# Kernel tuning notes

Hardware: AMD Instinct MI355X
Metric: run time of the kernel (lower is better)

## Reference

```python
import jax, jax.numpy as jnp
import numpy as np
from jax import lax

NF = 64
KS = 3
PAD = 1
TOPK = 2
DG = 8          # deformable_groups
N = KS * KS     # 9 sampling points


def conv3x3(x, w, b):
    y = lax.conv_general_dilated(x, w, (1, 1), 'SAME',
                                 dimension_numbers=('NCHW', 'OIHW', 'NCHW'))
    return y + b[None, :, None, None]


def lrelu(x):
    return jnp.where(x >= 0, x, 0.1 * x)


def dsp_sample(x, feat, w_om, b_om):
    """Modulated deformable sampling (DSP_sep2): returns the N bilinearly
    sampled, mask-modulated taps per pixel, shape (B, C, N, H, W)."""
    B, C, H, W = x.shape
    Cg = C // DG
    om = conv3x3(feat, w_om, b_om)              # (B, 3*DG*N, H, W)
    o1, o2, m = jnp.split(om, 3, axis=1)
    off_y = o1.reshape(B, DG, N, H, W)
    off_x = o2.reshape(B, DG, N, H, W)
    mask = jax.nn.sigmoid(m).reshape(B, DG, 1, N, H * W)
    kk = (jnp.arange(KS) - PAD).astype(jnp.float32)
    kdy = jnp.repeat(kk, KS)                    # (N,) kernel row offsets
    kdx = jnp.tile(kk, KS)                      # (N,) kernel col offsets
    ii = jnp.arange(H, dtype=jnp.float32)
    jj = jnp.arange(W, dtype=jnp.float32)
    ys = ii[None, None, None, :, None] + kdy[None, None, :, None, None] + off_y
    xs = jj[None, None, None, None, :] + kdx[None, None, :, None, None] + off_x
    y0 = jnp.floor(ys)
    x0 = jnp.floor(xs)
    xf = x.reshape(B, DG, Cg, H * W)
    out = jnp.zeros((B, DG, Cg, N, H * W), x.dtype)
    # bilinear interpolation with zero padding outside the image
    for dy in (0.0, 1.0):
        for dx in (0.0, 1.0):
            yi = y0 + dy
            xi = x0 + dx
            wgt = (1.0 - jnp.abs(ys - yi)) * (1.0 - jnp.abs(xs - xi))
            valid = (yi >= 0) & (yi <= H - 1) & (xi >= 0) & (xi <= W - 1)
            lin = (jnp.clip(yi, 0, H - 1) * W + jnp.clip(xi, 0, W - 1)).astype(jnp.int32)
            g = jnp.take_along_axis(xf[:, :, :, None, :],
                                    lin.reshape(B, DG, 1, N, H * W), axis=-1)
            out = out + g * jnp.where(valid, wgt, 0.0).reshape(B, DG, 1, N, H * W)
    return (out * mask).reshape(B, C, N, H, W)


def setup_inputs() -> dict:
    key = jax.random.key(0)
    ks = jax.random.split(key, 9)
    B, C, H, W = 2, NF, 192, 192

    def rn(k, s, sc=1.0):
        return jax.random.normal(k, s, jnp.float32) * sc

    return {
        'query': rn(ks[0], (B, C, H, W)),
        'key':   rn(ks[1], (B, C, H, W)),
        'value': rn(ks[2], (B, C, H, W)),
        'w1': rn(ks[3], (C, 2 * C, 3, 3), 0.05), 'b1': rn(ks[4], (C,), 0.05),
        'w2': rn(ks[5], (C, C, 3, 3), 0.05),     'b2': rn(ks[6], (C,), 0.05),
        'w_om': rn(ks[7], (3 * DG * N, C, 3, 3), 0.01),
        'b_om': rn(ks[8], (3 * DG * N,), 0.01),
    }


def reference(query, key, value, w1, b1, w2, b2, w_om, b_om):
    B, C, H, W = query.shape
    HW = H * W
    feat = lrelu(conv3x3(jnp.concatenate([query, key], axis=1), w1, b1))
    feat = lrelu(conv3x3(feat, w2, b2))
    # deformable sampled keys: (B, C, N, H, W) -> (B, HW, N, C)
    key_off = dsp_sample(key, feat, w_om, b_om).transpose(0, 3, 4, 2, 1).reshape(B, HW, N, C)
    q = query.reshape(B, C, HW).transpose(0, 2, 1)            # (B, HW, C)
    rel = jnp.einsum('bpnc,bpc->bpn', key_off, q)             # relevance scores
    topv, topi = lax.top_k(rel, TOPK)                         # (B, HW, TOPK)
    corr = jax.nn.softmax(topv, axis=-1)
    val_off = dsp_sample(value, feat, w_om, b_om).transpose(0, 3, 4, 2, 1).reshape(B, HW, N, C)
    k_sel = jnp.take_along_axis(key_off, topi[..., None], axis=2)  # (B, HW, TOPK, C)
    v_sel = jnp.take_along_axis(val_off, topi[..., None], axis=2)
    k_upd = jnp.einsum('bptc,bpt->bpc', k_sel, corr)
    v_out = jnp.einsum('bptc,bpt->bpc', v_sel, corr).transpose(0, 2, 1)  # (B, C, HW)
    weight = jnp.einsum('bpc,bpc->bp', q, k_upd)              # (B, HW)
    return (weight, v_out)
```

## Files before the change

kernel.cpp:

```cpp
#include <hip/hip_runtime.h>
#include <math.h>

#define H_  192
#define W_  192
#define HW_ (192 * 192)
#define B_  2
#define C_  64
#define PW_ 194

typedef __attribute__((ext_vector_type(8))) short short8;
typedef __attribute__((ext_vector_type(4))) short short4v;
typedef __attribute__((ext_vector_type(4))) float float4v;
typedef _Float16 __attribute__((ext_vector_type(8))) half8;

union hbits { _Float16 f; short s; };
__device__ __forceinline__ void split2(float x, short& h, short& l) {
    _Float16 hf = (_Float16)x;
    float r = (x - (float)hf) * 4096.f;
    _Float16 lf = (_Float16)r;
    hbits u;
    u.f = hf; h = u.s;
    u.f = lf; l = u.s;
}

__device__ __forceinline__ float bilin_dot(const float* __restrict__ pl,
                                           float ys, float xs, int c4,
                                           float4v q4) {
    float y0 = floorf(ys), x0 = floorf(xs);
    float fy = ys - y0, fx = xs - x0;
    int iy = (int)y0, ix = (int)x0;
    float acc = 0.f;
    #pragma unroll
    for (int dy = 0; dy < 2; ++dy) {
        #pragma unroll
        for (int dx = 0; dx < 2; ++dx) {
            int yy = iy + dy, xx = ix + dx;
            float wgt = (dy ? fy : 1.f - fy) * (dx ? fx : 1.f - fx);
            bool valid = (yy >= 0) && (yy < H_) && (xx >= 0) && (xx < W_);
            int yc = min(max(yy, 0), H_ - 1);
            int xc = min(max(xx, 0), W_ - 1);
            const float4v v = *(const float4v*)(pl + (size_t)(yc * W_ + xc) * 64 + c4);
            float d = v[0] * q4[0] + v[1] * q4[1] + v[2] * q4[2] + v[3] * q4[3];
            acc += valid ? wgt * d : 0.f;
        }
    }
    return acc;
}
__device__ __forceinline__ float4v bilin_v4(const float* __restrict__ pl,
                                            float ys, float xs, int c4) {
    float y0 = floorf(ys), x0 = floorf(xs);
    float fy = ys - y0, fx = xs - x0;
    int iy = (int)y0, ix = (int)x0;
    float4v acc;
    acc[0] = acc[1] = acc[2] = acc[3] = 0.f;
    #pragma unroll
    for (int dy = 0; dy < 2; ++dy) {
        #pragma unroll
        for (int dx = 0; dx < 2; ++dx) {
            int yy = iy + dy, xx = ix + dx;
            float wgt = (dy ? fy : 1.f - fy) * (dx ? fx : 1.f - fx);
            bool valid = (yy >= 0) && (yy < H_) && (xx >= 0) && (xx < W_);
            float wz = valid ? wgt : 0.f;
            int yc = min(max(yy, 0), H_ - 1);
            int xc = min(max(xx, 0), W_ - 1);
            const float4v v = *(const float4v*)(pl + (size_t)(yc * W_ + xc) * 64 + c4);
            #pragma unroll
            for (int r = 0; r < 4; ++r) acc[r] += wz * v[r];
        }
    }
    return acc;
}

__global__ __launch_bounds__(256) void prep_w_k(
    const float* __restrict__ w1, const float* __restrict__ w2,
    const float* __restrict__ wom,
    short* __restrict__ pw1, short* __restrict__ pw2, short* __restrict__ pwom)
{
    int idx = blockIdx.x * 256 + threadIdx.x;
    int arr;
    if (idx < 144 * 512) { arr = 0; }
    else if (idx < (144 + 72) * 512) { arr = 1; idx -= 144 * 512; }
    else if (idx < (144 + 72 + 252) * 512) { arr = 2; idx -= (144 + 72) * 512; }
    else return;
    int frag = idx >> 9, within = idx & 511;
    int lane = within >> 3, j = within & 7;
    int KS   = (arr == 0) ? 4 : 2;
    int mt   = frag / (9 * KS);
    int rem  = frag % (9 * KS);
    int kk   = rem / KS;
    int s    = rem % KS;
    int co   = mt * 16 + (lane & 15);
    int c    = s * 32 + (lane >> 4) * 8 + j;
    float v = 0.f;
    if (arr == 0)      v = w1[(co * 128 + c) * 9 + kk];
    else if (arr == 1) v = w2[(co * 64 + c) * 9 + kk];
    else if (co < 216) v = wom[(co * 64 + c) * 9 + kk];
    short h, l;
    split2(v, h, l);
    short* dst = (arr == 0) ? pw1 : (arr == 1) ? pw2 : pwom;
    size_t base = (size_t)frag * 1024 + lane * 8 + j;
    dst[base]       = h;
    dst[base + 512] = l;
}

__global__ __launch_bounds__(256) void pack_qk(
    const float* __restrict__ q, const float* __restrict__ k,
    short* __restrict__ qk2)
{
    __shared__ float sm[128][65];
    const int tid  = threadIdx.x;
    const int flat = blockIdx.x;
    const int xcd  = flat & 7;
    const int cc_  = flat >> 3;
    const int b    = xcd >> 2;
    const int r4   = xcd & 3;
    const int i    = r4 * 48 + cc_ / 3;
    const int j0   = (cc_ % 3) * 64;
    const int p0   = i * W_ + j0;
    const int pp   = tid & 63;
    const int r0   = tid >> 6;
    #pragma unroll
    for (int c = r0; c < 128; c += 4) {
        const float* src = (c < 64) ? q : k;
        sm[c][pp] = src[(size_t)(b * 64 + (c & 63)) * HW_ + p0 + pp];
    }
    __syncthreads();
    for (int idx = tid; idx < 64 * 128; idx += 256) {
        int pxw = idx >> 7, ci = idx & 127;
        short h, l;
        split2(sm[ci][pxw], h, l);
        short* dstp = qk2 + ((size_t)(b * PW_ + i + 1) * PW_ + j0 + pxw + 1) * 256;
        dstp[ci]       = h;
        dstp[128 + ci] = l;
    }
}

__global__ __launch_bounds__(256) void zero_borders(
    short* __restrict__ f1p, short* __restrict__ f2p, short* __restrict__ qk2)
{
    const int prow = blockIdx.x;
    const int b    = blockIdx.y;
    const int z    = blockIdx.z;
    short* dst = (z == 0) ? f1p : (z == 1) ? f2p : qk2;
    const int nc = (z == 2) ? 256 : 128;
    dst += (size_t)(b * PW_ + prow) * PW_ * nc;
    if (prow == 0 || prow == PW_ - 1) {
        for (int idx = threadIdx.x; idx < PW_ * nc; idx += 256) dst[idx] = 0;
    } else {
        for (int idx = threadIdx.x; idx < nc; idx += 256) {
            dst[idx] = 0;
            dst[(size_t)(PW_ - 1) * nc + idx] = 0;
        }
    }
}

__global__ __launch_bounds__(256) void nchw_to_nhwc(
    const float* __restrict__ key, const float* __restrict__ value,
    float* __restrict__ kT, float* __restrict__ vT)
{
    __shared__ float sm[64][65];
    const int tid = threadIdx.x;
    const int p0  = blockIdx.x * 64;
    const int b   = blockIdx.y;
    const float* src = blockIdx.z ? value : key;
    float*       dst = blockIdx.z ? vT    : kT;
    const int pp = tid & 63;
    const int r0 = tid >> 6;
    #pragma unroll
    for (int c = r0; c < 64; c += 4)
        sm[c][pp] = src[(size_t)(b * 64 + c) * HW_ + p0 + pp];
    __syncthreads();
    const int cc = tid & 63;
    #pragma unroll
    for (int pw = r0; pw < 64; pw += 4)
        dst[((size_t)b * HW_ + p0 + pw) * 64 + cc] = sm[cc][pw];
}

template<int CIN, int MT, bool LRELU, int OUTMODE>
__global__ __launch_bounds__(256) void conv_direct(
    const short* __restrict__ in, const short* __restrict__ pw,
    const float* __restrict__ bias, void* __restrict__ outv)
{
    constexpr int KS  = CIN / 32;
    constexpr int MTW = MT / 2;
    constexpr int NT  = 9 * KS;

    const int tid  = threadIdx.x;
    const int lane = tid & 63;
    const int w    = tid >> 6;
    const int wh   = w & 1;
    const int wn   = w >> 1;
    const int quad = lane >> 4;
    const int nn   = lane & 15;

    const int flat = blockIdx.x;
    const int xcd  = flat & 7;
    const int cc_  = flat >> 3;
    const int b    = xcd >> 2;
    const int r4   = xcd & 3;
    const int i    = r4 * 48 + cc_ / 3;
    const int j0   = (cc_ % 3) * 64;
    const int mt0  = wh * MTW;

    constexpr float CSC = 1.f / 4096.f;

    float4v accM[MTW][2];
    #pragma unroll
    for (int m = 0; m < MTW; ++m)
        #pragma unroll
        for (int t = 0; t < 2; ++t)
            #pragma unroll
            for (int r = 0; r < 4; ++r) accM[m][t][r] = 0.f;

    float4v zvec;
    zvec[0] = zvec[1] = zvec[2] = zvec[3] = 0.f;

    auto baddr = [&](int it, int t2) -> const short* {
        const int ky = it / (3 * KS);
        const int rm = it % (3 * KS);
        const int kx = rm / KS;
        const int s  = rm % KS;
        const int pcol = j0 + kx + (wn * 2 + t2) * 16 + nn;
        return in + ((size_t)(b * PW_ + i + ky) * PW_ + pcol) * (2 * CIN)
                  + s * 32 + quad * 8;
    };

    half8 bhc[2], blc[2];
    #pragma unroll
    for (int t2 = 0; t2 < 2; ++t2) {
        const short* bp = baddr(0, t2);
        bhc[t2] = *(const half8*)bp;
        blc[t2] = *(const half8*)(bp + CIN);
    }

    #pragma unroll
    for (int it = 0; it < NT; ++it) {
        half8 bhn[2], bln[2];
        if (it + 1 < NT) {
            #pragma unroll
            for (int t2 = 0; t2 < 2; ++t2) {
                const short* bp = baddr(it + 1, t2);
                bhn[t2] = *(const half8*)bp;
                bln[t2] = *(const half8*)(bp + CIN);
            }
        } else {
            #pragma unroll
            for (int t2 = 0; t2 < 2; ++t2) { bhn[t2] = bhc[t2]; bln[t2] = blc[t2]; }
        }

        const int ky = it / (3 * KS);
        const int rm = it % (3 * KS);
        const int kx = rm / KS;
        const int s  = rm % KS;
        const int kk = ky * 3 + kx;

        #pragma unroll
        for (int m = 0; m < MTW; ++m) {
            const short* ap = pw
                + ((size_t)(((mt0 + m) * 9 + kk) * KS + s)) * 1024
                + lane * 8;
            half8 ah = *(const half8*)ap;
            half8 al = *(const half8*)(ap + 512);
            float4v t0, t1;
            accM[m][0] = __builtin_amdgcn_mfma_f32_16x16x32_f16(ah, bhc[0], accM[m][0], 0, 0, 0);
            t0         = __builtin_amdgcn_mfma_f32_16x16x32_f16(ah, blc[0], zvec,       0, 0, 0);
            accM[m][1] = __builtin_amdgcn_mfma_f32_16x16x32_f16(ah, bhc[1], accM[m][1], 0, 0, 0);
            t1         = __builtin_amdgcn_mfma_f32_16x16x32_f16(ah, blc[1], zvec,       0, 0, 0);
            t0         = __builtin_amdgcn_mfma_f32_16x16x32_f16(al, bhc[0], t0,         0, 0, 0);
            t1         = __builtin_amdgcn_mfma_f32_16x16x32_f16(al, bhc[1], t1,         0, 0, 0);
            #pragma unroll
            for (int r = 0; r < 4; ++r) {
                accM[m][0][r] += t0[r] * CSC;
                accM[m][1][r] += t1[r] * CSC;
            }
        }

        #pragma unroll
        for (int t2 = 0; t2 < 2; ++t2) { bhc[t2] = bhn[t2]; blc[t2] = bln[t2]; }
    }

    #pragma unroll
    for (int m = 0; m < MTW; ++m) {
        const int co0 = (mt0 + m) * 16 + quad * 4;
        #pragma unroll
        for (int t2 = 0; t2 < 2; ++t2) {
            const int t = wn * 2 + t2;
            if (OUTMODE == 0) {
                const size_t pp = ((size_t)(b * PW_ + i + 1) * PW_
                                   + (j0 + t * 16 + nn + 1)) * 128;
                short* feat = (short*)outv;
                short4v hv, lv;
                #pragma unroll
                for (int r = 0; r < 4; ++r) {
                    float x = accM[m][t2][r] + bias[co0 + r];
                    if (LRELU) x = (x >= 0.f) ? x : 0.1f * x;
                    short h, l;
                    split2(x, h, l);
                    hv[r] = h; lv[r] = l;
                }
                *(short4v*)(feat + pp + co0)      = hv;
                *(short4v*)(feat + pp + 64 + co0) = lv;
            } else {
                if (co0 < 216) {
                    const int p = i * W_ + j0 + t * 16 + nn;
                    float* om = (float*)outv;
                    float4v v;
                    #pragma unroll
                    for (int r = 0; r < 4; ++r)
                        v[r] = accM[m][t2][r] + bias[co0 + r];
                    *(float4v*)(om + ((size_t)b * HW_ + p) * 216 + co0) = v;
                }
            }
        }
    }
}

__global__ __launch_bounds__(256) void sampler_k(
    const float* __restrict__ query, const float* __restrict__ kT,
    const float* __restrict__ vT, const float* __restrict__ om,
    float* __restrict__ out_w, float* __restrict__ out_v)
{
    __shared__ float sq[16 * 68];
    const int tid  = threadIdx.x;
    const int bb   = blockIdx.x;
    const int b    = bb / 2304;
    const int pblk = (bb - b * 2304) * 16;

    #pragma unroll
    for (int k = 0; k < 4; ++k) {
        int idx = tid + k * 256;
        int c   = idx >> 4;
        int px  = idx & 15;
        sq[px * 68 + c] = query[(size_t)(b * 64 + c) * HW_ + pblk + px];
    }
    __syncthreads();

    const int lane   = tid & 63;
    const int w      = tid >> 6;
    const int px_sub = lane >> 4;
    const int cl     = lane & 15;
    const int c4     = cl * 4;
    const int g      = cl >> 1;
    const int p      = pblk + w * 4 + px_sub;
    const int i      = p / W_;
    const int j      = p - i * W_;

    const float4v q4 = *(const float4v*)&sq[(w * 4 + px_sub) * 68 + c4];

    const float* omb = om + ((size_t)b * HW_ + p) * 216;
    float offy[9], offx[9], mk[9];
    #pragma unroll
    for (int n = 0; n < 9; ++n) {
        offy[n] = omb[g * 9 + n];
        offx[n] = omb[72 + g * 9 + n];
        float mv = omb[144 + g * 9 + n];
        mk[n] = 1.f / (1.f + expf(-mv));
    }

    const float* kpl = kT + (size_t)b * HW_ * 64;
    float rel[9];
    #pragma unroll
    for (int n = 0; n < 9; ++n) {
        float ys = (float)i + (float)(n / 3 - 1) + offy[n];
        float xs = (float)j + (float)(n % 3 - 1) + offx[n];
        float d = bilin_dot(kpl, ys, xs, c4, q4) * mk[n];
        #pragma unroll
        for (int off = 1; off < 16; off <<= 1)
            d += __shfl_xor(d, off, 64);
        rel[n] = d;
    }

    int n0 = 0; float v0 = rel[0];
    #pragma unroll
    for (int n = 1; n < 9; ++n) { if (rel[n] > v0) { v0 = rel[n]; n0 = n; } }
    int n1 = -1; float v1 = -1e30f;
    #pragma unroll
    for (int n = 0; n < 9; ++n) { if (n != n0 && rel[n] > v1) { v1 = rel[n]; n1 = n; } }

    float e1  = expf(v1 - v0);
    float inv = 1.f / (1.f + e1);
    float c0 = inv, c1 = e1 * inv;

    if (cl == 0) out_w[(size_t)b * HW_ + p] = c0 * v0 + c1 * v1;

    float oy0 = 0, ox0 = 0, m0 = 0, oy1 = 0, ox1 = 0, m1 = 0;
    #pragma unroll
    for (int n = 0; n < 9; ++n) {
        if (n == n0) { oy0 = offy[n]; ox0 = offx[n]; m0 = mk[n]; }
        if (n == n1) { oy1 = offy[n]; ox1 = offx[n]; m1 = mk[n]; }
    }

    const float* vpl = vT + (size_t)b * HW_ * 64;
    float ys0 = (float)i + (float)(n0 / 3 - 1) + oy0;
    float xs0 = (float)j + (float)(n0 % 3 - 1) + ox0;
    float ys1 = (float)i + (float)(n1 / 3 - 1) + oy1;
    float xs1 = (float)j + (float)(n1 % 3 - 1) + ox1;
    float4v vv0 = bilin_v4(vpl, ys0, xs0, c4);
    float4v vv1 = bilin_v4(vpl, ys1, xs1, c4);
    float w0 = c0 * m0, w1s = c1 * m1;
    #pragma unroll
    for (int r = 0; r < 4; ++r)
        out_v[(size_t)(b * C_ + c4 + r) * HW_ + p] = w0 * vv0[r] + w1s * vv1[r];
}

extern "C" void kernel_launch(void* const* d_in, const int* in_sizes, int n_in,
                              void* d_out, int out_size, void* d_ws, size_t ws_size,
                              hipStream_t stream)
{
    const float* query = (const float*)d_in[0];
    const float* key   = (const float*)d_in[1];
    const float* value = (const float*)d_in[2];
    const float* w1    = (const float*)d_in[3];
    const float* b1    = (const float*)d_in[4];
    const float* w2    = (const float*)d_in[5];
    const float* b2    = (const float*)d_in[6];
    const float* wom   = (const float*)d_in[7];
    const float* bom   = (const float*)d_in[8];
    float* out = (float*)d_out;

    char* ws = (char*)d_ws;
    float* om   = (float*)(ws);
    short* f1p  = (short*)(ws);
    short* qk2  = (short*)(ws + 19269632);
    short* pw1  = (short*)(ws + 57808896);
    short* pw2  = (short*)(ws + 58103808);
    short* f2p  = (short*)(ws + 63700992);
    short* pwom = (short*)(ws + 82970624);
    float* kT   = (float*)(ws + 63700992);
    float* vT   = (float*)(ws + 82575360);

    zero_borders<<<dim3(PW_, B_, 3), 256, 0, stream>>>(f1p, f2p, qk2);
    pack_qk<<<1152, 256, 0, stream>>>(query, key, qk2);
    prep_w_k<<<936, 256, 0, stream>>>(w1, w2, wom, pw1, pw2, pwom);

    conv_direct<128, 4,  true,  0><<<1152, 256, 0, stream>>>(qk2, pw1, b1, (void*)f1p);
    conv_direct<64,  4,  true,  0><<<1152, 256, 0, stream>>>(f1p, pw2, b2, (void*)f2p);
    conv_direct<64,  14, false, 1><<<1152, 256, 0, stream>>>(f2p, pwom, bom, (void*)om);

    nchw_to_nhwc<<<dim3(576, B_, 2), 256, 0, stream>>>(key, value, kT, vT);

    float* out_w = out;
    float* out_v = out + (size_t)B_ * HW_;
    sampler_k<<<(B_ * HW_) / 16, 256, 0, stream>>>(query, kT, vT, om, out_w, out_v);
}
```

Measured before the change: 462.2 us.

## Repartition conv warps so each wave owns all output tiles for one pixel strip

Each of the four waves in the direct-conv kernel now handles one 16-pixel column strip and all MT output-channel tiles. Previously the waves split channel tiles in halves and each covered two pixel strips. This halves the B-fragment (input) loads per wave and removes duplicated input traffic, at the cost of each wave loading every weight tile. A launch_bounds occupancy hint of 4 blocks is also added. The per-thread accumulator count stays the same.

```diff
diff --git a/kernel.cpp b/kernel.cpp
--- a/kernel.cpp
+++ b/kernel.cpp
@@ -177,19 +177,16 @@
 }
 
 template<int CIN, int MT, bool LRELU, int OUTMODE>
-__global__ __launch_bounds__(256) void conv_direct(
+__global__ __launch_bounds__(256, 4) void conv_direct(
     const short* __restrict__ in, const short* __restrict__ pw,
     const float* __restrict__ bias, void* __restrict__ outv)
 {
-    constexpr int KS  = CIN / 32;
-    constexpr int MTW = MT / 2;
-    constexpr int NT  = 9 * KS;
+    constexpr int KS = CIN / 32;
+    constexpr int NT = 9 * KS;
 
     const int tid  = threadIdx.x;
     const int lane = tid & 63;
-    const int w    = tid >> 6;
-    const int wh   = w & 1;
-    const int wn   = w >> 1;
+    const int wn   = tid >> 6;
     const int quad = lane >> 4;
     const int nn   = lane & 15;
 
@@ -200,53 +197,43 @@
     const int r4   = xcd & 3;
     const int i    = r4 * 48 + cc_ / 3;
     const int j0   = (cc_ % 3) * 64;
-    const int mt0  = wh * MTW;
 
     constexpr float CSC = 1.f / 4096.f;
 
-    float4v accM[MTW][2];
-    #pragma unroll
-    for (int m = 0; m < MTW; ++m)
+    float4v accM[MT];
+    #pragma unroll
+    for (int m = 0; m < MT; ++m)
         #pragma unroll
-        for (int t = 0; t < 2; ++t)
-            #pragma unroll
-            for (int r = 0; r < 4; ++r) accM[m][t][r] = 0.f;
+        for (int r = 0; r < 4; ++r) accM[m][r] = 0.f;
 
     float4v zvec;
     zvec[0] = zvec[1] = zvec[2] = zvec[3] = 0.f;
 
-    auto baddr = [&](int it, int t2) -> const short* {
+    auto baddr = [&](int it) -> const short* {
         const int ky = it / (3 * KS);
         const int rm = it % (3 * KS);
         const int kx = rm / KS;
         const int s  = rm % KS;
-        const int pcol = j0 + kx + (wn * 2 + t2) * 16 + nn;
+        const int pcol = j0 + kx + wn * 16 + nn;
         return in + ((size_t)(b * PW_ + i + ky) * PW_ + pcol) * (2 * CIN)
                   + s * 32 + quad * 8;
     };
 
-    half8 bhc[2], blc[2];
-    #pragma unroll
-    for (int t2 = 0; t2 < 2; ++t2) {
-        const short* bp = baddr(0, t2);
-        bhc[t2] = *(const half8*)bp;
-        blc[t2] = *(const half8*)(bp + CIN);
+    half8 bhc, blc;
+    {
+        const short* bp = baddr(0);
+        bhc = *(const half8*)bp;
+        blc = *(const half8*)(bp + CIN);
     }
 
     #pragma unroll
     for (int it = 0; it < NT; ++it) {
-        half8 bhn[2], bln[2];
+        half8 bhn, bln;
         if (it + 1 < NT) {
-            #pragma unroll
-            for (int t2 = 0; t2 < 2; ++t2) {
-                const short* bp = baddr(it + 1, t2);
-                bhn[t2] = *(const half8*)bp;
-                bln[t2] = *(const half8*)(bp + CIN);
-            }
-        } else {
-            #pragma unroll
-            for (int t2 = 0; t2 < 2; ++t2) { bhn[t2] = bhc[t2]; bln[t2] = blc[t2]; }
-        }
+            const short* bp = baddr(it + 1);
+            bhn = *(const half8*)bp;
+            bln = *(const half8*)(bp + CIN);
+        } else { bhn = bhc; bln = blc; }
 
         const int ky = it / (3 * KS);
         const int rm = it % (3 * KS);
@@ -255,61 +242,50 @@
         const int kk = ky * 3 + kx;
 
         #pragma unroll
-        for (int m = 0; m < MTW; ++m) {
+        for (int m = 0; m < MT; ++m) {
             const short* ap = pw
-                + ((size_t)(((mt0 + m) * 9 + kk) * KS + s)) * 1024
+                + ((size_t)((m * 9 + kk) * KS + s)) * 1024
                 + lane * 8;
             half8 ah = *(const half8*)ap;
             half8 al = *(const half8*)(ap + 512);
-            float4v t0, t1;
-            accM[m][0] = __builtin_amdgcn_mfma_f32_16x16x32_f16(ah, bhc[0], accM[m][0], 0, 0, 0);
-            t0         = __builtin_amdgcn_mfma_f32_16x16x32_f16(ah, blc[0], zvec,       0, 0, 0);
-            accM[m][1] = __builtin_amdgcn_mfma_f32_16x16x32_f16(ah, bhc[1], accM[m][1], 0, 0, 0);
-            t1         = __builtin_amdgcn_mfma_f32_16x16x32_f16(ah, blc[1], zvec,       0, 0, 0);
-            t0         = __builtin_amdgcn_mfma_f32_16x16x32_f16(al, bhc[0], t0,         0, 0, 0);
-            t1         = __builtin_amdgcn_mfma_f32_16x16x32_f16(al, bhc[1], t1,         0, 0, 0);
+            float4v t0;
+            accM[m] = __builtin_amdgcn_mfma_f32_16x16x32_f16(ah, bhc, accM[m], 0, 0, 0);
+            t0      = __builtin_amdgcn_mfma_f32_16x16x32_f16(ah, blc, zvec,    0, 0, 0);
+            t0      = __builtin_amdgcn_mfma_f32_16x16x32_f16(al, bhc, t0,      0, 0, 0);
+            #pragma unroll
+            for (int r = 0; r < 4; ++r) accM[m][r] += t0[r] * CSC;
+        }
+
+        bhc = bhn; blc = bln;
+    }
+
+    #pragma unroll
+    for (int m = 0; m < MT; ++m) {
+        const int co0 = m * 16 + quad * 4;
+        if (OUTMODE == 0) {
+            const size_t pp = ((size_t)(b * PW_ + i + 1) * PW_
+                               + (j0 + wn * 16 + nn + 1)) * 128;
+            short* feat = (short*)outv;
+            short4v hv, lv;
             #pragma unroll
             for (int r = 0; r < 4; ++r) {
-                accM[m][0][r] += t0[r] * CSC;
-                accM[m][1][r] += t1[r] * CSC;
+                float x = accM[m][r] + bias[co0 + r];
+                if (LRELU) x = (x >= 0.f) ? x : 0.1f * x;
+                short h, l;
+                split2(x, h, l);
+                hv[r] = h; lv[r] = l;
             }
-        }
-
-        #pragma unroll
-        for (int t2 = 0; t2 < 2; ++t2) { bhc[t2] = bhn[t2]; blc[t2] = bln[t2]; }
-    }
-
-    #pragma unroll
-    for (int m = 0; m < MTW; ++m) {
-        const int co0 = (mt0 + m) * 16 + quad * 4;
-        #pragma unroll
-        for (int t2 = 0; t2 < 2; ++t2) {
-            const int t = wn * 2 + t2;
-            if (OUTMODE == 0) {
-                const size_t pp = ((size_t)(b * PW_ + i + 1) * PW_
-                                   + (j0 + t * 16 + nn + 1)) * 128;
-                short* feat = (short*)outv;
-                short4v hv, lv;
+            *(short4v*)(feat + pp + co0)      = hv;
+            *(short4v*)(feat + pp + 64 + co0) = lv;
+        } else {
+            if (co0 < 216) {
+                const int p = i * W_ + j0 + wn * 16 + nn;
+                float* om = (float*)outv;
+                float4v v;
                 #pragma unroll
-                for (int r = 0; r < 4; ++r) {
-                    float x = accM[m][t2][r] + bias[co0 + r];
-                    if (LRELU) x = (x >= 0.f) ? x : 0.1f * x;
-                    short h, l;
-                    split2(x, h, l);
-                    hv[r] = h; lv[r] = l;
-                }
-                *(short4v*)(feat + pp + co0)      = hv;
-                *(short4v*)(feat + pp + 64 + co0) = lv;
-            } else {
-                if (co0 < 216) {
-                    const int p = i * W_ + j0 + t * 16 + nn;
-                    float* om = (float*)outv;
-                    float4v v;
-                    #pragma unroll
-                    for (int r = 0; r < 4; ++r)
-                        v[r] = accM[m][t2][r] + bias[co0 + r];
-                    *(float4v*)(om + ((size_t)b * HW_ + p) * 216 + co0) = v;
-                }
+                for (int r = 0; r < 4; ++r)
+                    v[r] = accM[m][r] + bias[co0 + r];
+                *(float4v*)(om + ((size_t)b * HW_ + p) * 216 + co0) = v;
             }
         }
     }
```

Result: slower. 556.0 us (+20.3%).
